# Kernel optimization log

Measured on AMD Instinct MI355X. Metric: run time of the kernel, lower is better.

## Reference

```python
import jax, jax.numpy as jnp
import numpy as np

N_NODES, N_EDGES = 20000, 400000
IN_DIM, HC, OUT_DIM, EDGE_DIM = 128, 128, 128, 2


def _add_self_loops(src, dst, ea, n):
    # PyG fill_value='mean': self-loop edge_attr = mean of incoming edge_attr
    deg = jax.ops.segment_sum(jnp.ones(src.shape[0], ea.dtype), dst, num_segments=n)
    mean_ea = jax.ops.segment_sum(ea, dst, num_segments=n) / jnp.clip(deg, 1.0)[:, None]
    loop = jnp.arange(n, dtype=src.dtype)
    return (jnp.concatenate([src, loop]), jnp.concatenate([dst, loop]),
            jnp.concatenate([ea, mean_ea], axis=0))


def _gat(x, src, dst, ea, W, att_s, att_d, We, att_e, b, heads, out_ch, concat):
    n = x.shape[0]
    xh = (x @ W).reshape(n, heads, out_ch)                      # [N,H,C]
    a_src = jnp.einsum('nhc,hc->nh', xh, att_s)                  # [N,H]
    a_dst = jnp.einsum('nhc,hc->nh', xh, att_d)
    eh = (ea @ We).reshape(-1, heads, out_ch)                    # [E,H,C]
    a_e = jnp.einsum('ehc,hc->eh', eh, att_e)                    # [E,H]
    alpha = jax.nn.leaky_relu(a_src[src] + a_dst[dst] + a_e, 0.2)
    # segment softmax over destination nodes (every node has a self loop)
    amax = jax.ops.segment_max(alpha, dst, num_segments=n)
    amax = jnp.where(jnp.isfinite(amax), amax, 0.0)
    ex = jnp.exp(alpha - amax[dst])
    denom = jax.ops.segment_sum(ex, dst, num_segments=n)
    w = ex / (denom[dst] + 1e-16)                                # [E,H]
    out = jax.ops.segment_sum(xh[src] * w[..., None], dst, num_segments=n)  # [N,H,C]
    out = out.reshape(n, heads * out_ch) if concat else out.mean(axis=1)
    return out + b


def setup_inputs() -> dict:
    key = jax.random.key(0)
    ks = jax.random.split(key, 16)
    g = lambda k, shape, fan: jax.random.normal(k, shape, jnp.float32) * (1.0 / np.sqrt(fan))
    inp = {
        'x': jax.random.normal(ks[0], (N_NODES, IN_DIM), jnp.float32),
        'edge_index': jax.random.randint(ks[1], (2, N_EDGES), 0, N_NODES, jnp.int32),
        'edge_attr': jax.random.normal(ks[2], (N_EDGES, EDGE_DIM), jnp.float32),
        # conv1: GATConv(128 -> hc=128, heads=2, edge_dim=2, concat=True)
        'W1': g(ks[3], (IN_DIM, 2 * HC), IN_DIM),
        'att_s1': g(ks[4], (2, HC), HC),
        'att_d1': g(ks[5], (2, HC), HC),
        'We1': g(ks[6], (EDGE_DIM, 2 * HC), EDGE_DIM),
        'att_e1': g(ks[7], (2, HC), HC),
        'b1': jnp.zeros((2 * HC,), jnp.float32),
        # conv2: GATConv(256 -> 128, heads=1, edge_dim=2, concat=False)
        'W2': g(ks[8], (2 * HC, OUT_DIM), 2 * HC),
        'att_s2': g(ks[9], (1, OUT_DIM), OUT_DIM),
        'att_d2': g(ks[10], (1, OUT_DIM), OUT_DIM),
        'We2': g(ks[11], (EDGE_DIM, OUT_DIM), EDGE_DIM),
        'att_e2': g(ks[12], (1, OUT_DIM), OUT_DIM),
        'b2': jnp.zeros((OUT_DIM,), jnp.float32),
    }
    return inp


def reference(x, edge_index, edge_attr, W1, att_s1, att_d1, We1, att_e1, b1,
              W2, att_s2, att_d2, We2, att_e2, b2):
    n = x.shape[0]
    src0, dst0 = edge_index[0], edge_index[1]
    src, dst, ea = _add_self_loops(src0, dst0, edge_attr, n)
    x0 = x
    h = jax.nn.relu(_gat(x, src, dst, ea, W1, att_s1, att_d1, We1, att_e1, b1,
                         heads=2, out_ch=HC, concat=True))
    h = _gat(h, src, dst, ea, W2, att_s2, att_d2, We2, att_e2, b2,
             heads=1, out_ch=OUT_DIM, concat=False)
    # SimpleConv(aggr='mean'): mean over incoming neighbors on the ORIGINAL edges
    deg = jax.ops.segment_sum(jnp.ones(src0.shape[0], h.dtype), dst0, num_segments=n)
    mean_h = jax.ops.segment_sum(h[src0], dst0, num_segments=n) / jnp.clip(deg, 1.0)[:, None]
    return jax.nn.relu(mean_h + x0)
```

## Files before the change

kernel.cpp:

```cpp
#include <hip/hip_runtime.h>
#include <hip/hip_bf16.h>

#define NN 20000
#define NE 400000
#define SLOTS 64

typedef unsigned short u16;
typedef unsigned int u32;
typedef unsigned long long u64;

typedef __attribute__((ext_vector_type(8))) short bf16x8;
typedef __attribute__((ext_vector_type(4))) float f32x4;

__device__ __forceinline__ float bf2f(u16 u) {
    union { u32 i; float f; } v; v.i = ((u32)u) << 16; return v.f;
}
__device__ __forceinline__ u16 f2bf(float f) {
    __hip_bfloat16 h = __float2bfloat16(f);
    return *reinterpret_cast<u16*>(&h);
}
__device__ __forceinline__ u32 pack2(float lo, float hi) {
    return (u32)f2bf(lo) | ((u32)f2bf(hi) << 16);
}

struct us4 { u16 x, y, z, w; };

__global__ void k_pre(const float* __restrict__ We1, const float* __restrict__ att_e1,
                      const float* __restrict__ We2, const float* __restrict__ att_e2,
                      int* __restrict__ cnt, float* __restrict__ consts) {
    int i = blockIdx.x * 256 + threadIdx.x;
    if (i < NN) cnt[i] = 0;
    if (blockIdx.x == 0) {
        __shared__ float red[128];
        int c = threadIdx.x;
        float p[6];
        if (c < 128) {
            p[0] = We1[0 * 256 + 0 * 128 + c] * att_e1[0 * 128 + c];
            p[1] = We1[0 * 256 + 1 * 128 + c] * att_e1[1 * 128 + c];
            p[2] = We1[1 * 256 + 0 * 128 + c] * att_e1[0 * 128 + c];
            p[3] = We1[1 * 256 + 1 * 128 + c] * att_e1[1 * 128 + c];
            p[4] = We2[0 * 128 + c] * att_e2[c];
            p[5] = We2[1 * 128 + c] * att_e2[c];
        }
        for (int j = 0; j < 6; j++) {
            if (c < 128) red[c] = p[j];
            __syncthreads();
            for (int off = 64; off >= 1; off >>= 1) {
                if (c < off) red[c] += red[c + off];
                __syncthreads();
            }
            if (c == 0) consts[j] = red[0];
            __syncthreads();
        }
    }
}

__global__ void k_build(const int* __restrict__ ei, const float* __restrict__ ea,
                        const float* __restrict__ consts, int* __restrict__ cnt,
                        int* __restrict__ slotS, float2* __restrict__ slotA1,
                        float* __restrict__ slotA2) {
    int e = blockIdx.x * 256 + threadIdx.x;
    if (e >= NE) return;
    int d = ei[NE + e];
    int s = ei[e];
    float2 v = *reinterpret_cast<const float2*>(ea + (size_t)e * 2);
    int pos = atomicAdd(&cnt[d], 1);
    if (pos < SLOTS) {
        slotS[d * SLOTS + pos] = s;
        slotA1[d * SLOTS + pos] = make_float2(v.x * consts[0] + v.y * consts[2],
                                              v.x * consts[1] + v.y * consts[3]);
        slotA2[d * SLOTS + pos] = v.x * consts[4] + v.y * consts[5];
    }
}

__global__ void k_prep_w(const float* __restrict__ W1, const float* __restrict__ W2,
                         u16* __restrict__ Bt1, u16* __restrict__ Bt2) {
    int idx = blockIdx.x * 256 + threadIdx.x;
    if (idx < 32768) {
        int n = idx >> 7, k = idx & 127;
        Bt1[idx] = f2bf(W1[k * 256 + n]);
    } else {
        int j = idx - 32768;
        int n = j >> 8, k = j & 255;
        Bt2[j] = f2bf(W2[k * 128 + n]);
    }
}

__global__ __launch_bounds__(256) void k_gemm1(const float* __restrict__ A,
                                               const u16* __restrict__ Bt,
                                               const float* __restrict__ att_s,
                                               const float* __restrict__ att_d,
                                               u16* __restrict__ C,
                                               float2* __restrict__ a_s,
                                               float2* __restrict__ a_d) {
    constexpr int K = 128, KC = 4, NT = 16;
    int lane = threadIdx.x & 63;
    int wave = threadIdx.x >> 6;
    int r0 = (blockIdx.x * 4 + wave) * 16;
    if (r0 >= NN) return;
    int mrow = lane & 15, g = lane >> 4;
    int arow = r0 + mrow; if (arow >= NN) arow = NN - 1;
    const float* abase = A + (size_t)arow * K + g * 8;
    bf16x8 a[KC];
#pragma unroll
    for (int kc = 0; kc < KC; kc++) {
        float4 lo = *reinterpret_cast<const float4*>(abase + kc * 32);
        float4 hi = *reinterpret_cast<const float4*>(abase + kc * 32 + 4);
        bf16x8 t;
        t[0] = (short)f2bf(lo.x); t[1] = (short)f2bf(lo.y);
        t[2] = (short)f2bf(lo.z); t[3] = (short)f2bf(lo.w);
        t[4] = (short)f2bf(hi.x); t[5] = (short)f2bf(hi.y);
        t[6] = (short)f2bf(hi.z); t[7] = (short)f2bf(hi.w);
        a[kc] = t;
    }
    f32x4 acc[NT];
#pragma unroll
    for (int nt = 0; nt < NT; nt++) acc[nt] = (f32x4){0.f, 0.f, 0.f, 0.f};
#pragma unroll
    for (int nt = 0; nt < NT; nt++) {
        const u16* bbase = Bt + (size_t)(nt * 16 + mrow) * K + g * 8;
#pragma unroll
        for (int kc = 0; kc < KC; kc++) {
            bf16x8 b = *reinterpret_cast<const bf16x8*>(bbase + kc * 32);
            acc[nt] = __builtin_amdgcn_mfma_f32_16x16x32_bf16(a[kc], b, acc[nt], 0, 0, 0);
        }
    }
    int orow0 = r0 + g * 4;
#pragma unroll
    for (int nt = 0; nt < NT; nt++)
#pragma unroll
        for (int r = 0; r < 4; r++) {
            int rr = orow0 + r;
            if (rr < NN) C[(size_t)rr * 256 + nt * 16 + mrow] = f2bf(acc[nt][r]);
        }
    float attsv[NT], attdv[NT];
#pragma unroll
    for (int nt = 0; nt < NT; nt++) {
        attsv[nt] = att_s[nt * 16 + mrow];
        attdv[nt] = att_d[nt * 16 + mrow];
    }
#pragma unroll
    for (int r = 0; r < 4; r++) {
        float s0 = 0.f, s1 = 0.f, d0 = 0.f, d1 = 0.f;
#pragma unroll
        for (int nt = 0; nt < 8; nt++) { s0 += acc[nt][r] * attsv[nt]; d0 += acc[nt][r] * attdv[nt]; }
#pragma unroll
        for (int nt = 8; nt < NT; nt++) { s1 += acc[nt][r] * attsv[nt]; d1 += acc[nt][r] * attdv[nt]; }
        for (int off = 8; off >= 1; off >>= 1) {
            s0 += __shfl_xor(s0, off); s1 += __shfl_xor(s1, off);
            d0 += __shfl_xor(d0, off); d1 += __shfl_xor(d1, off);
        }
        int rr = orow0 + r;
        if (mrow == 0 && rr < NN) {
            a_s[rr] = make_float2(s0, s1);
            a_d[rr] = make_float2(d0, d1);
        }
    }
}

__global__ __launch_bounds__(256) void k_gemm2(const u16* __restrict__ A,
                                               const u16* __restrict__ Bt,
                                               const float* __restrict__ att_s,
                                               const float* __restrict__ att_d,
                                               u16* __restrict__ C,
                                               float* __restrict__ a_s,
                                               float* __restrict__ a_d) {
    constexpr int K = 256, KC = 8, NT = 8;
    int lane = threadIdx.x & 63;
    int wave = threadIdx.x >> 6;
    int r0 = (blockIdx.x * 4 + wave) * 16;
    if (r0 >= NN) return;
    int mrow = lane & 15, g = lane >> 4;
    int arow = r0 + mrow; if (arow >= NN) arow = NN - 1;
    const u16* abase = A + (size_t)arow * K + g * 8;
    bf16x8 a[KC];
#pragma unroll
    for (int kc = 0; kc < KC; kc++) a[kc] = *reinterpret_cast<const bf16x8*>(abase + kc * 32);
    f32x4 acc[NT];
#pragma unroll
    for (int nt = 0; nt < NT; nt++) acc[nt] = (f32x4){0.f, 0.f, 0.f, 0.f};
#pragma unroll
    for (int nt = 0; nt < NT; nt++) {
        const u16* bbase = Bt + (size_t)(nt * 16 + mrow) * K + g * 8;
#pragma unroll
        for (int kc = 0; kc < KC; kc++) {
            bf16x8 b = *reinterpret_cast<const bf16x8*>(bbase + kc * 32);
            acc[nt] = __builtin_amdgcn_mfma_f32_16x16x32_bf16(a[kc], b, acc[nt], 0, 0, 0);
        }
    }
    int orow0 = r0 + g * 4;
#pragma unroll
    for (int nt = 0; nt < NT; nt++)
#pragma unroll
        for (int r = 0; r < 4; r++) {
            int rr = orow0 + r;
            if (rr < NN) C[(size_t)rr * 128 + nt * 16 + mrow] = f2bf(acc[nt][r]);
        }
    float attsv[NT], attdv[NT];
#pragma unroll
    for (int nt = 0; nt < NT; nt++) {
        attsv[nt] = att_s[nt * 16 + mrow];
        attdv[nt] = att_d[nt * 16 + mrow];
    }
#pragma unroll
    for (int r = 0; r < 4; r++) {
        float s0 = 0.f, d0 = 0.f;
#pragma unroll
        for (int nt = 0; nt < NT; nt++) { s0 += acc[nt][r] * attsv[nt]; d0 += acc[nt][r] * attdv[nt]; }
        for (int off = 8; off >= 1; off >>= 1) {
            s0 += __shfl_xor(s0, off);
            d0 += __shfl_xor(d0, off);
        }
        int rr = orow0 + r;
        if (mrow == 0 && rr < NN) { a_s[rr] = s0; a_d[rr] = d0; }
    }
}

__global__ __launch_bounds__(256) void k_conv1(const int* __restrict__ cnt,
                                               const int* __restrict__ slotS,
                                               const float2* __restrict__ slotA1,
                                               const u16* __restrict__ xh1,
                                               const float2* __restrict__ a_s,
                                               const float2* __restrict__ a_d,
                                               const float* __restrict__ b1,
                                               u16* __restrict__ h1out) {
    int lane = threadIdx.x & 63;
    int n = blockIdx.x * 4 + (threadIdx.x >> 6);
    if (n >= NN) return;
    int deg = cnt[n]; if (deg > SLOTS) deg = SLOTS;
    float2 ad = a_d[n];
    float2 asn = a_s[n];
    bool valid = lane < deg;
    int s = 0; float ae0 = 0.f, ae1 = 0.f;
    if (valid) {
        s = slotS[n * SLOTS + lane];
        float2 ev = slotA1[n * SLOTS + lane];
        ae0 = ev.x; ae1 = ev.y;
    }
    float sum0 = ae0, sum1 = ae1;
    for (int off = 32; off >= 1; off >>= 1) {
        sum0 += __shfl_xor(sum0, off);
        sum1 += __shfl_xor(sum1, off);
    }
    float invdeg = 1.f / (float)(deg < 1 ? 1 : deg);
    float sae0 = sum0 * invdeg, sae1 = sum1 * invdeg;
    float2 asv = valid ? a_s[s] : make_float2(0.f, 0.f);
    float l0 = asv.x + ad.x + ae0;
    float l1 = asv.y + ad.y + ae1;
    l0 = l0 >= 0.f ? l0 : 0.2f * l0;
    l1 = l1 >= 0.f ? l1 : 0.2f * l1;
    if (!valid) { l0 = -3.4e38f; l1 = -3.4e38f; }
    float sl0 = asn.x + ad.x + sae0;
    float sl1 = asn.y + ad.y + sae1;
    sl0 = sl0 >= 0.f ? sl0 : 0.2f * sl0;
    sl1 = sl1 >= 0.f ? sl1 : 0.2f * sl1;
    float cm0 = l0, cm1 = l1;
    for (int off = 32; off >= 1; off >>= 1) {
        cm0 = fmaxf(cm0, __shfl_xor(cm0, off));
        cm1 = fmaxf(cm1, __shfl_xor(cm1, off));
    }
    float m0 = fmaxf(cm0, sl0), m1 = fmaxf(cm1, sl1);
    float e0 = valid ? __expf(l0 - m0) : 0.f;
    float e1 = valid ? __expf(l1 - m1) : 0.f;
    float es0 = __expf(sl0 - m0), es1 = __expf(sl1 - m1);
    float cs0 = e0, cs1 = e1;
    for (int off = 32; off >= 1; off >>= 1) {
        cs0 += __shfl_xor(cs0, off);
        cs1 += __shfl_xor(cs1, off);
    }
    float den0 = cs0 + es0 + 1e-16f, den1 = cs1 + es1 + 1e-16f;
    int half = lane >> 5, hl = lane & 31;
    int ch = hl * 8;
    int myh = hl >> 4;
    float acc0 = 0.f, acc1 = 0.f, acc2 = 0.f, acc3 = 0.f;
    float acc4 = 0.f, acc5 = 0.f, acc6 = 0.f, acc7 = 0.f;
    for (int j = 0; j < deg; j += 2) {
        int jj = j + half;
        bool ve = jj < deg;
        int sj = ve ? __shfl(s, jj) : n;
        float w0 = __shfl(e0, jj), w1 = __shfl(e1, jj);
        float wj = ve ? (myh ? w1 : w0) : 0.f;
        uint4 v = *reinterpret_cast<const uint4*>(xh1 + (size_t)sj * 256 + ch);
        acc0 += wj * bf2f((u16)(v.x & 0xffff));
        acc1 += wj * bf2f((u16)(v.x >> 16));
        acc2 += wj * bf2f((u16)(v.y & 0xffff));
        acc3 += wj * bf2f((u16)(v.y >> 16));
        acc4 += wj * bf2f((u16)(v.z & 0xffff));
        acc5 += wj * bf2f((u16)(v.z >> 16));
        acc6 += wj * bf2f((u16)(v.w & 0xffff));
        acc7 += wj * bf2f((u16)(v.w >> 16));
    }
    acc0 += __shfl_xor(acc0, 32); acc1 += __shfl_xor(acc1, 32);
    acc2 += __shfl_xor(acc2, 32); acc3 += __shfl_xor(acc3, 32);
    acc4 += __shfl_xor(acc4, 32); acc5 += __shfl_xor(acc5, 32);
    acc6 += __shfl_xor(acc6, 32); acc7 += __shfl_xor(acc7, 32);
    if (half == 0) {
        float ws = myh ? es1 : es0;
        uint4 v = *reinterpret_cast<const uint4*>(xh1 + (size_t)n * 256 + ch);
        acc0 += ws * bf2f((u16)(v.x & 0xffff));
        acc1 += ws * bf2f((u16)(v.x >> 16));
        acc2 += ws * bf2f((u16)(v.y & 0xffff));
        acc3 += ws * bf2f((u16)(v.y >> 16));
        acc4 += ws * bf2f((u16)(v.z & 0xffff));
        acc5 += ws * bf2f((u16)(v.z >> 16));
        acc6 += ws * bf2f((u16)(v.w & 0xffff));
        acc7 += ws * bf2f((u16)(v.w >> 16));
        float inv = 1.f / (myh ? den1 : den0);
        float4 ba = *reinterpret_cast<const float4*>(b1 + ch);
        float4 bb = *reinterpret_cast<const float4*>(b1 + ch + 4);
        float o0 = acc0 * inv + ba.x, o1 = acc1 * inv + ba.y;
        float o2 = acc2 * inv + ba.z, o3 = acc3 * inv + ba.w;
        float o4 = acc4 * inv + bb.x, o5 = acc5 * inv + bb.y;
        float o6 = acc6 * inv + bb.z, o7 = acc7 * inv + bb.w;
        uint4 st;
        st.x = pack2(o0 > 0.f ? o0 : 0.f, o1 > 0.f ? o1 : 0.f);
        st.y = pack2(o2 > 0.f ? o2 : 0.f, o3 > 0.f ? o3 : 0.f);
        st.z = pack2(o4 > 0.f ? o4 : 0.f, o5 > 0.f ? o5 : 0.f);
        st.w = pack2(o6 > 0.f ? o6 : 0.f, o7 > 0.f ? o7 : 0.f);
        *reinterpret_cast<uint4*>(h1out + (size_t)n * 256 + ch) = st;
    }
}

__global__ __launch_bounds__(256) void k_conv2(const int* __restrict__ cnt,
                                               const int* __restrict__ slotS,
                                               const float* __restrict__ slotA2,
                                               const u16* __restrict__ xh2,
                                               const float* __restrict__ a_s,
                                               const float* __restrict__ a_d,
                                               const float* __restrict__ b2v,
                                               u16* __restrict__ h2out) {
    int lane = threadIdx.x & 63;
    int n = blockIdx.x * 4 + (threadIdx.x >> 6);
    if (n >= NN) return;
    int deg = cnt[n]; if (deg > SLOTS) deg = SLOTS;
    float ad = a_d[n];
    float asn = a_s[n];
    bool valid = lane < deg;
    int s = 0; float ae = 0.f;
    if (valid) {
        s = slotS[n * SLOTS + lane];
        ae = slotA2[n * SLOTS + lane];
    }
    float sum = ae;
    for (int off = 32; off >= 1; off >>= 1) sum += __shfl_xor(sum, off);
    float invdeg = 1.f / (float)(deg < 1 ? 1 : deg);
    float sae = sum * invdeg;
    float l = (valid ? a_s[s] : 0.f) + ad + ae;
    l = l >= 0.f ? l : 0.2f * l;
    if (!valid) l = -3.4e38f;
    float sl = asn + ad + sae;
    sl = sl >= 0.f ? sl : 0.2f * sl;
    float cm = l;
    for (int off = 32; off >= 1; off >>= 1) cm = fmaxf(cm, __shfl_xor(cm, off));
    float m = fmaxf(cm, sl);
    float e = valid ? __expf(l - m) : 0.f;
    float es = __expf(sl - m);
    float cs = e;
    for (int off = 32; off >= 1; off >>= 1) cs += __shfl_xor(cs, off);
    float den = cs + es + 1e-16f;
    int half = lane >> 5, hl = lane & 31;
    int ch = hl * 4;
    float acc0 = 0.f, acc1 = 0.f, acc2 = 0.f, acc3 = 0.f;
    for (int j = 0; j < deg; j += 2) {
        int jj = j + half;
        bool ve = jj < deg;
        int sj = ve ? __shfl(s, jj) : n;
        float wj = ve ? __shfl(e, jj) : 0.f;
        uint2 v = *reinterpret_cast<const uint2*>(xh2 + (size_t)sj * 128 + ch);
        acc0 += wj * bf2f((u16)(v.x & 0xffff));
        acc1 += wj * bf2f((u16)(v.x >> 16));
        acc2 += wj * bf2f((u16)(v.y & 0xffff));
        acc3 += wj * bf2f((u16)(v.y >> 16));
    }
    acc0 += __shfl_xor(acc0, 32); acc1 += __shfl_xor(acc1, 32);
    acc2 += __shfl_xor(acc2, 32); acc3 += __shfl_xor(acc3, 32);
    if (half == 0) {
        uint2 v = *reinterpret_cast<const uint2*>(xh2 + (size_t)n * 128 + ch);
        acc0 += es * bf2f((u16)(v.x & 0xffff));
        acc1 += es * bf2f((u16)(v.x >> 16));
        acc2 += es * bf2f((u16)(v.y & 0xffff));
        acc3 += es * bf2f((u16)(v.y >> 16));
        float inv = 1.f / den;
        float4 b4 = *reinterpret_cast<const float4*>(b2v + ch);
        uint2 st;
        st.x = pack2(acc0 * inv + b4.x, acc1 * inv + b4.y);
        st.y = pack2(acc2 * inv + b4.z, acc3 * inv + b4.w);
        *reinterpret_cast<uint2*>(h2out + (size_t)n * 128 + ch) = st;
    }
}

__global__ __launch_bounds__(256) void k_final(const int* __restrict__ cnt,
                                               const int* __restrict__ slotS,
                                               const u16* __restrict__ h2,
                                               const float* __restrict__ x,
                                               float* __restrict__ out) {
    int lane = threadIdx.x & 63;
    int n = blockIdx.x * 4 + (threadIdx.x >> 6);
    if (n >= NN) return;
    int deg = cnt[n]; if (deg > SLOTS) deg = SLOTS;
    int s = (lane < deg) ? slotS[n * SLOTS + lane] : 0;
    int half = lane >> 5, hl = lane & 31;
    int ch = hl * 4;
    float acc0 = 0.f, acc1 = 0.f, acc2 = 0.f, acc3 = 0.f;
    for (int j = 0; j < deg; j += 2) {
        int jj = j + half;
        bool ve = jj < deg;
        int sj = ve ? __shfl(s, jj) : n;
        float wj = ve ? 1.f : 0.f;
        uint2 v = *reinterpret_cast<const uint2*>(h2 + (size_t)sj * 128 + ch);
        acc0 += wj * bf2f((u16)(v.x & 0xffff));
        acc1 += wj * bf2f((u16)(v.x >> 16));
        acc2 += wj * bf2f((u16)(v.y & 0xffff));
        acc3 += wj * bf2f((u16)(v.y >> 16));
    }
    acc0 += __shfl_xor(acc0, 32); acc1 += __shfl_xor(acc1, 32);
    acc2 += __shfl_xor(acc2, 32); acc3 += __shfl_xor(acc3, 32);
    if (half == 0) {
        float invd = 1.f / (float)(deg < 1 ? 1 : deg);
        float4 xv = *reinterpret_cast<const float4*>(x + (size_t)n * 128 + ch);
        float o0 = acc0 * invd + xv.x;
        float o1 = acc1 * invd + xv.y;
        float o2 = acc2 * invd + xv.z;
        float o3 = acc3 * invd + xv.w;
        float4 st = make_float4(o0 > 0.f ? o0 : 0.f, o1 > 0.f ? o1 : 0.f,
                                o2 > 0.f ? o2 : 0.f, o3 > 0.f ? o3 : 0.f);
        *reinterpret_cast<float4*>(out + (size_t)n * 128 + ch) = st;
    }
}

extern "C" void kernel_launch(void* const* d_in, const int* in_sizes, int n_in,
                              void* d_out, int out_size, void* d_ws, size_t ws_size,
                              hipStream_t stream) {
    const float* x      = (const float*)d_in[0];
    const int*   ei     = (const int*)d_in[1];
    const float* ea     = (const float*)d_in[2];
    const float* W1     = (const float*)d_in[3];
    const float* att_s1 = (const float*)d_in[4];
    const float* att_d1 = (const float*)d_in[5];
    const float* We1    = (const float*)d_in[6];
    const float* att_e1 = (const float*)d_in[7];
    const float* b1     = (const float*)d_in[8];
    const float* W2     = (const float*)d_in[9];
    const float* att_s2 = (const float*)d_in[10];
    const float* att_d2 = (const float*)d_in[11];
    const float* We2    = (const float*)d_in[12];
    const float* att_e2 = (const float*)d_in[13];
    const float* b2     = (const float*)d_in[14];
    float* out = (float*)d_out;

    char* w = (char*)d_ws;
    auto alloc = [&](size_t bytes) -> void* {
        void* p = (void*)w;
        w += (bytes + 255) & ~(size_t)255;
        return p;
    };
    int*    cnt    = (int*)alloc(NN * 4);
    float*  consts = (float*)alloc(64);
    int*    slotS  = (int*)alloc((size_t)NN * SLOTS * 4);
    float2* slotA1 = (float2*)alloc((size_t)NN * SLOTS * 8);
    float*  slotA2 = (float*)alloc((size_t)NN * SLOTS * 4);
    u16*    Bt1    = (u16*)alloc(256 * 128 * 2);
    u16*    Bt2    = (u16*)alloc(128 * 256 * 2);
    u16*    xh1b   = (u16*)alloc((size_t)NN * 256 * 2);
    u16*    h1b    = (u16*)alloc((size_t)NN * 256 * 2);
    float2* a_s1   = (float2*)alloc(NN * 8);
    float2* a_d1   = (float2*)alloc(NN * 8);
    float*  a_s2   = (float*)alloc(NN * 4);
    float*  a_d2   = (float*)alloc(NN * 4);
    u16* xh2b = xh1b;
    u16* h2b  = h1b;

    k_pre<<<(NN + 255) / 256, 256, 0, stream>>>(We1, att_e1, We2, att_e2, cnt, consts);
    k_build<<<(NE + 255) / 256, 256, 0, stream>>>(ei, ea, consts, cnt, slotS, slotA1, slotA2);
    k_prep_w<<<(65536 + 255) / 256, 256, 0, stream>>>(W1, W2, Bt1, Bt2);

    k_gemm1<<<(NN + 63) / 64, 256, 0, stream>>>(x, Bt1, att_s1, att_d1, xh1b, a_s1, a_d1);
    k_conv1<<<(NN + 3) / 4, 256, 0, stream>>>(cnt, slotS, slotA1, xh1b, a_s1, a_d1, b1, h1b);
    k_gemm2<<<(NN + 63) / 64, 256, 0, stream>>>(h1b, Bt2, att_s2, att_d2, xh2b, a_s2, a_d2);
    k_conv2<<<(NN + 3) / 4, 256, 0, stream>>>(cnt, slotS, slotA2, xh2b, a_s2, a_d2, b2, h2b);
    k_final<<<(NN + 3) / 4, 256, 0, stream>>>(cnt, slotS, h2b, x, out);
}
```

Before: 163.0 us.

## Pack slot arrays into float4 records, widen gather to 4 edges per wave

Result: faster. 142.9 us (-12.3%).

```diff
diff --git a/kernel.cpp b/kernel.cpp
--- a/kernel.cpp
+++ b/kernel.cpp
@@ -23,13 +23,21 @@
     return (u32)f2bf(lo) | ((u32)f2bf(hi) << 16);
 }
 
-struct us4 { u16 x, y, z, w; };
-
 __global__ void k_pre(const float* __restrict__ We1, const float* __restrict__ att_e1,
                       const float* __restrict__ We2, const float* __restrict__ att_e2,
-                      int* __restrict__ cnt, float* __restrict__ consts) {
-    int i = blockIdx.x * 256 + threadIdx.x;
-    if (i < NN) cnt[i] = 0;
+                      const float* __restrict__ W1, const float* __restrict__ W2,
+                      int* __restrict__ cnt, float* __restrict__ consts,
+                      u16* __restrict__ Bt1, u16* __restrict__ Bt2) {
+    int idx = blockIdx.x * 256 + threadIdx.x;
+    if (idx < NN) cnt[idx] = 0;
+    if (idx < 32768) {
+        int n = idx >> 7, k = idx & 127;
+        Bt1[idx] = f2bf(W1[k * 256 + n]);
+    } else {
+        int j = idx - 32768;
+        int n = j >> 8, k = j & 255;
+        Bt2[j] = f2bf(W2[k * 128 + n]);
+    }
     if (blockIdx.x == 0) {
         __shared__ float red[128];
         int c = threadIdx.x;
@@ -57,8 +65,7 @@
 
 __global__ void k_build(const int* __restrict__ ei, const float* __restrict__ ea,
                         const float* __restrict__ consts, int* __restrict__ cnt,
-                        int* __restrict__ slotS, float2* __restrict__ slotA1,
-                        float* __restrict__ slotA2) {
+                        float4* __restrict__ slot) {
     int e = blockIdx.x * 256 + threadIdx.x;
     if (e >= NE) return;
     int d = ei[NE + e];
@@ -66,23 +73,12 @@
     float2 v = *reinterpret_cast<const float2*>(ea + (size_t)e * 2);
     int pos = atomicAdd(&cnt[d], 1);
     if (pos < SLOTS) {
-        slotS[d * SLOTS + pos] = s;
-        slotA1[d * SLOTS + pos] = make_float2(v.x * consts[0] + v.y * consts[2],
-                                              v.x * consts[1] + v.y * consts[3]);
-        slotA2[d * SLOTS + pos] = v.x * consts[4] + v.y * consts[5];
-    }
-}
-
-__global__ void k_prep_w(const float* __restrict__ W1, const float* __restrict__ W2,
-                         u16* __restrict__ Bt1, u16* __restrict__ Bt2) {
-    int idx = blockIdx.x * 256 + threadIdx.x;
-    if (idx < 32768) {
-        int n = idx >> 7, k = idx & 127;
-        Bt1[idx] = f2bf(W1[k * 256 + n]);
-    } else {
-        int j = idx - 32768;
-        int n = j >> 8, k = j & 255;
-        Bt2[j] = f2bf(W2[k * 128 + n]);
+        float4 rec;
+        rec.x = __int_as_float(s);
+        rec.y = v.x * consts[0] + v.y * consts[2];
+        rec.z = v.x * consts[1] + v.y * consts[3];
+        rec.w = v.x * consts[4] + v.y * consts[5];
+        slot[d * SLOTS + pos] = rec;
     }
 }
 
@@ -217,8 +213,7 @@
 }
 
 __global__ __launch_bounds__(256) void k_conv1(const int* __restrict__ cnt,
-                                               const int* __restrict__ slotS,
-                                               const float2* __restrict__ slotA1,
+                                               const float4* __restrict__ slot,
                                                const u16* __restrict__ xh1,
                                                const float2* __restrict__ a_s,
                                                const float2* __restrict__ a_d,
@@ -233,9 +228,9 @@
     bool valid = lane < deg;
     int s = 0; float ae0 = 0.f, ae1 = 0.f;
     if (valid) {
-        s = slotS[n * SLOTS + lane];
-        float2 ev = slotA1[n * SLOTS + lane];
-        ae0 = ev.x; ae1 = ev.y;
+        float4 rec = slot[n * SLOTS + lane];
+        s = __float_as_int(rec.x);
+        ae0 = rec.y; ae1 = rec.z;
     }
     float sum0 = ae0, sum1 = ae1;
     for (int off = 32; off >= 1; off >>= 1) {
@@ -269,61 +264,72 @@
         cs1 += __shfl_xor(cs1, off);
     }
     float den0 = cs0 + es0 + 1e-16f, den1 = cs1 + es1 + 1e-16f;
-    int half = lane >> 5, hl = lane & 31;
-    int ch = hl * 8;
-    int myh = hl >> 4;
-    float acc0 = 0.f, acc1 = 0.f, acc2 = 0.f, acc3 = 0.f;
-    float acc4 = 0.f, acc5 = 0.f, acc6 = 0.f, acc7 = 0.f;
-    for (int j = 0; j < deg; j += 2) {
-        int jj = j + half;
+    int q = lane >> 4, ql = lane & 15;
+    int ch = ql * 16;
+    int myh = ql >> 3;
+    float acc[16];
+#pragma unroll
+    for (int i = 0; i < 16; i++) acc[i] = 0.f;
+    for (int j = 0; j < deg; j += 4) {
+        int jj = j + q;
         bool ve = jj < deg;
         int sj = ve ? __shfl(s, jj) : n;
         float w0 = __shfl(e0, jj), w1 = __shfl(e1, jj);
         float wj = ve ? (myh ? w1 : w0) : 0.f;
-        uint4 v = *reinterpret_cast<const uint4*>(xh1 + (size_t)sj * 256 + ch);
-        acc0 += wj * bf2f((u16)(v.x & 0xffff));
-        acc1 += wj * bf2f((u16)(v.x >> 16));
-        acc2 += wj * bf2f((u16)(v.y & 0xffff));
-        acc3 += wj * bf2f((u16)(v.y >> 16));
-        acc4 += wj * bf2f((u16)(v.z & 0xffff));
-        acc5 += wj * bf2f((u16)(v.z >> 16));
-        acc6 += wj * bf2f((u16)(v.w & 0xffff));
-        acc7 += wj * bf2f((u16)(v.w >> 16));
-    }
-    acc0 += __shfl_xor(acc0, 32); acc1 += __shfl_xor(acc1, 32);
-    acc2 += __shfl_xor(acc2, 32); acc3 += __shfl_xor(acc3, 32);
-    acc4 += __shfl_xor(acc4, 32); acc5 += __shfl_xor(acc5, 32);
-    acc6 += __shfl_xor(acc6, 32); acc7 += __shfl_xor(acc7, 32);
-    if (half == 0) {
+        const u16* p = xh1 + (size_t)sj * 256 + ch;
+        uint4 va = *reinterpret_cast<const uint4*>(p);
+        uint4 vb = *reinterpret_cast<const uint4*>(p + 8);
+        acc[0] += wj * bf2f((u16)(va.x & 0xffff)); acc[1] += wj * bf2f((u16)(va.x >> 16));
+        acc[2] += wj * bf2f((u16)(va.y & 0xffff)); acc[3] += wj * bf2f((u16)(va.y >> 16));
+        acc[4] += wj * bf2f((u16)(va.z & 0xffff)); acc[5] += wj * bf2f((u16)(va.z >> 16));
+        acc[6] += wj * bf2f((u16)(va.w & 0xffff)); acc[7] += wj * bf2f((u16)(va.w >> 16));
+        acc[8] += wj * bf2f((u16)(vb.x & 0xffff)); acc[9] += wj * bf2f((u16)(vb.x >> 16));
+        acc[10] += wj * bf2f((u16)(vb.y & 0xffff)); acc[11] += wj * bf2f((u16)(vb.y >> 16));
+        acc[12] += wj * bf2f((u16)(vb.z & 0xffff)); acc[13] += wj * bf2f((u16)(vb.z >> 16));
+        acc[14] += wj * bf2f((u16)(vb.w & 0xffff)); acc[15] += wj * bf2f((u16)(vb.w >> 16));
+    }
+#pragma unroll
+    for (int i = 0; i < 16; i++) {
+        acc[i] += __shfl_xor(acc[i], 16);
+        acc[i] += __shfl_xor(acc[i], 32);
+    }
+    if (q == 0) {
         float ws = myh ? es1 : es0;
-        uint4 v = *reinterpret_cast<const uint4*>(xh1 + (size_t)n * 256 + ch);
-        acc0 += ws * bf2f((u16)(v.x & 0xffff));
-        acc1 += ws * bf2f((u16)(v.x >> 16));
-        acc2 += ws * bf2f((u16)(v.y & 0xffff));
-        acc3 += ws * bf2f((u16)(v.y >> 16));
-        acc4 += ws * bf2f((u16)(v.z & 0xffff));
-        acc5 += ws * bf2f((u16)(v.z >> 16));
-        acc6 += ws * bf2f((u16)(v.w & 0xffff));
-        acc7 += ws * bf2f((u16)(v.w >> 16));
+        const u16* p = xh1 + (size_t)n * 256 + ch;
+        uint4 va = *reinterpret_cast<const uint4*>(p);
+        uint4 vb = *reinterpret_cast<const uint4*>(p + 8);
+        acc[0] += ws * bf2f((u16)(va.x & 0xffff)); acc[1] += ws * bf2f((u16)(va.x >> 16));
+        acc[2] += ws * bf2f((u16)(va.y & 0xffff)); acc[3] += ws * bf2f((u16)(va.y >> 16));
+        acc[4] += ws * bf2f((u16)(va.z & 0xffff)); acc[5] += ws * bf2f((u16)(va.z >> 16));
+        acc[6] += ws * bf2f((u16)(va.w & 0xffff)); acc[7] += ws * bf2f((u16)(va.w >> 16));
+        acc[8] += ws * bf2f((u16)(vb.x & 0xffff)); acc[9] += ws * bf2f((u16)(vb.x >> 16));
+        acc[10] += ws * bf2f((u16)(vb.y & 0xffff)); acc[11] += ws * bf2f((u16)(vb.y >> 16));
+        acc[12] += ws * bf2f((u16)(vb.z & 0xffff)); acc[13] += ws * bf2f((u16)(vb.z >> 16));
+        acc[14] += ws * bf2f((u16)(vb.w & 0xffff)); acc[15] += ws * bf2f((u16)(vb.w >> 16));
         float inv = 1.f / (myh ? den1 : den0);
-        float4 ba = *reinterpret_cast<const float4*>(b1 + ch);
-        float4 bb = *reinterpret_cast<const float4*>(b1 + ch + 4);
-        float o0 = acc0 * inv + ba.x, o1 = acc1 * inv + ba.y;
-        float o2 = acc2 * inv + ba.z, o3 = acc3 * inv + ba.w;
-        float o4 = acc4 * inv + bb.x, o5 = acc5 * inv + bb.y;
-        float o6 = acc6 * inv + bb.z, o7 = acc7 * inv + bb.w;
-        uint4 st;
-        st.x = pack2(o0 > 0.f ? o0 : 0.f, o1 > 0.f ? o1 : 0.f);
-        st.y = pack2(o2 > 0.f ? o2 : 0.f, o3 > 0.f ? o3 : 0.f);
-        st.z = pack2(o4 > 0.f ? o4 : 0.f, o5 > 0.f ? o5 : 0.f);
-        st.w = pack2(o6 > 0.f ? o6 : 0.f, o7 > 0.f ? o7 : 0.f);
-        *reinterpret_cast<uint4*>(h1out + (size_t)n * 256 + ch) = st;
+        float o[16];
+#pragma unroll
+        for (int i = 0; i < 4; i++) {
+            float4 b4 = *reinterpret_cast<const float4*>(b1 + ch + i * 4);
+            o[i * 4 + 0] = acc[i * 4 + 0] * inv + b4.x;
+            o[i * 4 + 1] = acc[i * 4 + 1] * inv + b4.y;
+            o[i * 4 + 2] = acc[i * 4 + 2] * inv + b4.z;
+            o[i * 4 + 3] = acc[i * 4 + 3] * inv + b4.w;
+        }
+#pragma unroll
+        for (int i = 0; i < 16; i++) o[i] = o[i] > 0.f ? o[i] : 0.f;
+        uint4 sa, sb;
+        sa.x = pack2(o[0], o[1]);  sa.y = pack2(o[2], o[3]);
+        sa.z = pack2(o[4], o[5]);  sa.w = pack2(o[6], o[7]);
+        sb.x = pack2(o[8], o[9]);  sb.y = pack2(o[10], o[11]);
+        sb.z = pack2(o[12], o[13]); sb.w = pack2(o[14], o[15]);
+        *reinterpret_cast<uint4*>(h1out + (size_t)n * 256 + ch) = sa;
+        *reinterpret_cast<uint4*>(h1out + (size_t)n * 256 + ch + 8) = sb;
     }
 }
 
 __global__ __launch_bounds__(256) void k_conv2(const int* __restrict__ cnt,
-                                               const int* __restrict__ slotS,
-                                               const float* __restrict__ slotA2,
+                                               const float4* __restrict__ slot,
                                                const u16* __restrict__ xh2,
                                                const float* __restrict__ a_s,
                                                const float* __restrict__ a_d,
@@ -338,8 +344,9 @@
     bool valid = lane < deg;
     int s = 0; float ae = 0.f;
     if (valid) {
-        s = slotS[n * SLOTS + lane];
-        ae = slotA2[n * SLOTS + lane];
+        float4 rec = slot[n * SLOTS + lane];
+        s = __float_as_int(rec.x);
+        ae = rec.w;
     }
     float sum = ae;
     for (int off = 32; off >= 1; off >>= 1) sum += __shfl_xor(sum, off);
@@ -358,39 +365,47 @@
     float cs = e;
     for (int off = 32; off >= 1; off >>= 1) cs += __shfl_xor(cs, off);
     float den = cs + es + 1e-16f;
-    int half = lane >> 5, hl = lane & 31;
-    int ch = hl * 4;
-    float acc0 = 0.f, acc1 = 0.f, acc2 = 0.f, acc3 = 0.f;
-    for (int j = 0; j < deg; j += 2) {
-        int jj = j + half;
+    int q = lane >> 4, ql = lane & 15;
+    int ch = ql * 8;
+    float acc[8];
+#pragma unroll
+    for (int i = 0; i < 8; i++) acc[i] = 0.f;
+    for (int j = 0; j < deg; j += 4) {
+        int jj = j + q;
         bool ve = jj < deg;
         int sj = ve ? __shfl(s, jj) : n;
         float wj = ve ? __shfl(e, jj) : 0.f;
-        uint2 v = *reinterpret_cast<const uint2*>(xh2 + (size_t)sj * 128 + ch);
-        acc0 += wj * bf2f((u16)(v.x & 0xffff));
-        acc1 += wj * bf2f((u16)(v.x >> 16));
-        acc2 += wj * bf2f((u16)(v.y & 0xffff));
-        acc3 += wj * bf2f((u16)(v.y >> 16));
-    }
-    acc0 += __shfl_xor(acc0, 32); acc1 += __shfl_xor(acc1, 32);
-    acc2 += __shfl_xor(acc2, 32); acc3 += __shfl_xor(acc3, 32);
-    if (half == 0) {
-        uint2 v = *reinterpret_cast<const uint2*>(xh2 + (size_t)n * 128 + ch);
-        acc0 += es * bf2f((u16)(v.x & 0xffff));
-        acc1 += es * bf2f((u16)(v.x >> 16));
-        acc2 += es * bf2f((u16)(v.y & 0xffff));
-        acc3 += es * bf2f((u16)(v.y >> 16));
+        uint4 v = *reinterpret_cast<const uint4*>(xh2 + (size_t)sj * 128 + ch);
+        acc[0] += wj * bf2f((u16)(v.x & 0xffff)); acc[1] += wj * bf2f((u16)(v.x >> 16));
+        acc[2] += wj * bf2f((u16)(v.y & 0xffff)); acc[3] += wj * bf2f((u16)(v.y >> 16));
+        acc[4] += wj * bf2f((u16)(v.z & 0xffff)); acc[5] += wj * bf2f((u16)(v.z >> 16));
+        acc[6] += wj * bf2f((u16)(v.w & 0xffff)); acc[7] += wj * bf2f((u16)(v.w >> 16));
+    }
+#pragma unroll
+    for (int i = 0; i < 8; i++) {
+        acc[i] += __shfl_xor(acc[i], 16);
+        acc[i] += __shfl_xor(acc[i], 32);
+    }
+    if (q == 0) {
+        uint4 v = *reinterpret_cast<const uint4*>(xh2 + (size_t)n * 128 + ch);
+        acc[0] += es * bf2f((u16)(v.x & 0xffff)); acc[1] += es * bf2f((u16)(v.x >> 16));
+        acc[2] += es * bf2f((u16)(v.y & 0xffff)); acc[3] += es * bf2f((u16)(v.y >> 16));
+        acc[4] += es * bf2f((u16)(v.z & 0xffff)); acc[5] += es * bf2f((u16)(v.z >> 16));
+        acc[6] += es * bf2f((u16)(v.w & 0xffff)); acc[7] += es * bf2f((u16)(v.w >> 16));
         float inv = 1.f / den;
-        float4 b4 = *reinterpret_cast<const float4*>(b2v + ch);
-        uint2 st;
-        st.x = pack2(acc0 * inv + b4.x, acc1 * inv + b4.y);
-        st.y = pack2(acc2 * inv + b4.z, acc3 * inv + b4.w);
-        *reinterpret_cast<uint2*>(h2out + (size_t)n * 128 + ch) = st;
+        float4 ba = *reinterpret_cast<const float4*>(b2v + ch);
+        float4 bb = *reinterpret_cast<const float4*>(b2v + ch + 4);
+        uint4 st;
+        st.x = pack2(acc[0] * inv + ba.x, acc[1] * inv + ba.y);
+        st.y = pack2(acc[2] * inv + ba.z, acc[3] * inv + ba.w);
+        st.z = pack2(acc[4] * inv + bb.x, acc[5] * inv + bb.y);
+        st.w = pack2(acc[6] * inv + bb.z, acc[7] * inv + bb.w);
+        *reinterpret_cast<uint4*>(h2out + (size_t)n * 128 + ch) = st;
     }
 }
 
 __global__ __launch_bounds__(256) void k_final(const int* __restrict__ cnt,
-                                               const int* __restrict__ slotS,
+                                               const float4* __restrict__ slot,
                                                const u16* __restrict__ h2,
                                                const float* __restrict__ x,
                                                float* __restrict__ out) {
@@ -398,33 +413,42 @@
     int n = blockIdx.x * 4 + (threadIdx.x >> 6);
     if (n >= NN) return;
     int deg = cnt[n]; if (deg > SLOTS) deg = SLOTS;
-    int s = (lane < deg) ? slotS[n * SLOTS + lane] : 0;
-    int half = lane >> 5, hl = lane & 31;
-    int ch = hl * 4;
-    float acc0 = 0.f, acc1 = 0.f, acc2 = 0.f, acc3 = 0.f;
-    for (int j = 0; j < deg; j += 2) {
-        int jj = j + half;
+    int s = (lane < deg) ? __float_as_int(slot[n * SLOTS + lane].x) : 0;
+    int q = lane >> 4, ql = lane & 15;
+    int ch = ql * 8;
+    float acc[8];
+#pragma unroll
+    for (int i = 0; i < 8; i++) acc[i] = 0.f;
+    for (int j = 0; j < deg; j += 4) {
+        int jj = j + q;
         bool ve = jj < deg;
         int sj = ve ? __shfl(s, jj) : n;
         float wj = ve ? 1.f : 0.f;
-        uint2 v = *reinterpret_cast<const uint2*>(h2 + (size_t)sj * 128 + ch);
-        acc0 += wj * bf2f((u16)(v.x & 0xffff));
-        acc1 += wj * bf2f((u16)(v.x >> 16));
-        acc2 += wj * bf2f((u16)(v.y & 0xffff));
-        acc3 += wj * bf2f((u16)(v.y >> 16));
-    }
-    acc0 += __shfl_xor(acc0, 32); acc1 += __shfl_xor(acc1, 32);
-    acc2 += __shfl_xor(acc2, 32); acc3 += __shfl_xor(acc3, 32);
-    if (half == 0) {
+        uint4 v = *reinterpret_cast<const uint4*>(h2 + (size_t)sj * 128 + ch);
+        acc[0] += wj * bf2f((u16)(v.x & 0xffff)); acc[1] += wj * bf2f((u16)(v.x >> 16));
+        acc[2] += wj * bf2f((u16)(v.y & 0xffff)); acc[3] += wj * bf2f((u16)(v.y >> 16));
+        acc[4] += wj * bf2f((u16)(v.z & 0xffff)); acc[5] += wj * bf2f((u16)(v.z >> 16));
+        acc[6] += wj * bf2f((u16)(v.w & 0xffff)); acc[7] += wj * bf2f((u16)(v.w >> 16));
+    }
+#pragma unroll
+    for (int i = 0; i < 8; i++) {
+        acc[i] += __shfl_xor(acc[i], 16);
+        acc[i] += __shfl_xor(acc[i], 32);
+    }
+    if (q == 0) {
         float invd = 1.f / (float)(deg < 1 ? 1 : deg);
-        float4 xv = *reinterpret_cast<const float4*>(x + (size_t)n * 128 + ch);
-        float o0 = acc0 * invd + xv.x;
-        float o1 = acc1 * invd + xv.y;
-        float o2 = acc2 * invd + xv.z;
-        float o3 = acc3 * invd + xv.w;
-        float4 st = make_float4(o0 > 0.f ? o0 : 0.f, o1 > 0.f ? o1 : 0.f,
+        float4 xa = *reinterpret_cast<const float4*>(x + (size_t)n * 128 + ch);
+        float4 xb = *reinterpret_cast<const float4*>(x + (size_t)n * 128 + ch + 4);
+        float o0 = acc[0] * invd + xa.x, o1 = acc[1] * invd + xa.y;
+        float o2 = acc[2] * invd + xa.z, o3 = acc[3] * invd + xa.w;
+        float o4 = acc[4] * invd + xb.x, o5 = acc[5] * invd + xb.y;
+        float o6 = acc[6] * invd + xb.z, o7 = acc[7] * invd + xb.w;
+        float4 sa = make_float4(o0 > 0.f ? o0 : 0.f, o1 > 0.f ? o1 : 0.f,
                                 o2 > 0.f ? o2 : 0.f, o3 > 0.f ? o3 : 0.f);
-        *reinterpret_cast<float4*>(out + (size_t)n * 128 + ch) = st;
+        float4 sb = make_float4(o4 > 0.f ? o4 : 0.f, o5 > 0.f ? o5 : 0.f,
+                                o6 > 0.f ? o6 : 0.f, o7 > 0.f ? o7 : 0.f);
+        *reinterpret_cast<float4*>(out + (size_t)n * 128 + ch) = sa;
+        *reinterpret_cast<float4*>(out + (size_t)n * 128 + ch + 4) = sb;
     }
 }
 
@@ -456,9 +480,7 @@
     };
     int*    cnt    = (int*)alloc(NN * 4);
     float*  consts = (float*)alloc(64);
-    int*    slotS  = (int*)alloc((size_t)NN * SLOTS * 4);
-    float2* slotA1 = (float2*)alloc((size_t)NN * SLOTS * 8);
-    float*  slotA2 = (float*)alloc((size_t)NN * SLOTS * 4);
+    float4* slot   = (float4*)alloc((size_t)NN * SLOTS * 16);
     u16*    Bt1    = (u16*)alloc(256 * 128 * 2);
     u16*    Bt2    = (u16*)alloc(128 * 256 * 2);
     u16*    xh1b   = (u16*)alloc((size_t)NN * 256 * 2);
@@ -470,13 +492,12 @@
     u16* xh2b = xh1b;
     u16* h2b  = h1b;
 
-    k_pre<<<(NN + 255) / 256, 256, 0, stream>>>(We1, att_e1, We2, att_e2, cnt, consts);
-    k_build<<<(NE + 255) / 256, 256, 0, stream>>>(ei, ea, consts, cnt, slotS, slotA1, slotA2);
-    k_prep_w<<<(65536 + 255) / 256, 256, 0, stream>>>(W1, W2, Bt1, Bt2);
+    k_pre<<<256, 256, 0, stream>>>(We1, att_e1, We2, att_e2, W1, W2, cnt, consts, Bt1, Bt2);
+    k_build<<<(NE + 255) / 256, 256, 0, stream>>>(ei, ea, consts, cnt, slot);
 
     k_gemm1<<<(NN + 63) / 64, 256, 0, stream>>>(x, Bt1, att_s1, att_d1, xh1b, a_s1, a_d1);
-    k_conv1<<<(NN + 3) / 4, 256, 0, stream>>>(cnt, slotS, slotA1, xh1b, a_s1, a_d1, b1, h1b);
+    k_conv1<<<(NN + 3) / 4, 256, 0, stream>>>(cnt, slot, xh1b, a_s1, a_d1, b1, h1b);
     k_gemm2<<<(NN + 63) / 64, 256, 0, stream>>>(h1b, Bt2, att_s2, att_d2, xh2b, a_s2, a_d2);
-    k_conv2<<<(NN + 3) / 4, 256, 0, stream>>>(cnt, slotS, slotA2, xh2b, a_s2, a_d2, b2, h2b);
-    k_final<<<(NN + 3) / 4, 256, 0, stream>>>(cnt, slotS, h2b, x, out);
-}
+    k_conv2<<<(NN + 3) / 4, 256, 0, stream>>>(cnt, slot, xh2b, a_s2, a_d2, b2, h2b);
+    k_final<<<(NN + 3) / 4, 256, 0, stream>>>(cnt, slot, h2b, x, out);
+}
```
